# Kernel tuning notes

Hardware: AMD Instinct MI355X
Metric: run time of the kernel (lower is better)

The kernel has to match this reference:

```python
import jax, jax.numpy as jnp
import numpy as np

# Dimensions (see shape_source)
B, L, H, NH = 4, 1024, 768, 12      # batch, seq len, hidden, attention heads
E, MPE, K = 32, 4, 16               # entities/doc, mentions per entity, link spans/doc
EM = E * MPE                        # total mentions per doc
TYPE_DIM = 20
OFFSET = 1                          # bert-style [CLS] offset


def setup_inputs() -> dict:
    key = jax.random.key(0)
    ks = jax.random.split(key, 6)
    sequence_output = jax.random.normal(ks[0], (B, L, H), jnp.float32)
    attention = jax.random.uniform(ks[1], (B, NH, L, L), jnp.float32)
    type_table = jax.random.normal(ks[2], (3, TYPE_DIM), jnp.float32)
    mention_pos = jax.random.randint(ks[3], (B, E, MPE), 0, L - 2)
    link_start = jax.random.randint(ks[4], (B, K), 0, L - 64)
    link_len = jax.random.randint(ks[5], (B, K), 0, 31)
    return dict(sequence_output=sequence_output, attention=attention,
                type_table=type_table, mention_pos=mention_pos,
                link_start=link_start, link_len=link_len)


def reference(sequence_output, attention, type_table, mention_pos, link_start, link_len):
    dt = sequence_output.dtype
    # ---- mention gather (make_graph): mention node = token emb at start+offset ----
    pos = (mention_pos + OFFSET).reshape(B, EM)                       # [B,EM]
    m_emb = jnp.take_along_axis(sequence_output, pos[:, :, None], axis=1)  # [B,EM,H]
    # attention rows at mention positions: [B,NH,EM,L]
    mention_att = jax.vmap(lambda a, p: a[:, p])(attention, pos)
    # ---- entity pooling: logsumexp of member mention embs, mean of their att rows ----
    entity_emb = jax.nn.logsumexp(m_emb.reshape(B, E, MPE, H), axis=2)      # [B,E,H]
    entity_att = mention_att.reshape(B, NH, E, MPE, L).mean(axis=3)         # [B,NH,E,L]
    # ---- link span pooling: mean over rows of (head-mean att[s:e,s:e]) @ seq[s:e] ----
    att_h = attention.mean(axis=1)                                          # [B,L,L]
    s = link_start + OFFSET
    e = link_start + link_len + 1 + OFFSET                                  # span len >= 1
    r = jnp.arange(L)
    mask = ((r[None, None, :] >= s[:, :, None]) & (r[None, None, :] < e[:, :, None])).astype(dt)  # [B,K,L]
    length = (e - s).astype(dt)[:, :, None]
    w = jnp.einsum('bkr,brc->bkc', mask, att_h) * mask                      # row-summed span att
    link_rep = jnp.einsum('bkc,bch->bkh', w, sequence_output) / length      # [B,K,H]
    # ---- node bank: [entities | mentions | links] + type embedding ----
    nodes_raw = jnp.concatenate([entity_emb, m_emb, link_rep], axis=1)      # [B,N,H]
    type_ids = jnp.concatenate([jnp.zeros(E, jnp.int32), jnp.ones(EM, jnp.int32),
                                jnp.full((K,), 2, jnp.int32)])
    nodes_type = jnp.broadcast_to(type_table[type_ids][None], (B, E + EM + K, TYPE_DIM))
    nodes = jnp.concatenate([nodes_raw, nodes_type], axis=-1)               # [B,N,H+20]
    # ---- relation_map: attention-weighted context pooling over the document ----
    e_att = entity_att.mean(axis=1)                                         # [B,E,L] head-mean
    e_att = e_att / (e_att.sum(axis=-1, keepdims=True) + 1e-5)
    e_context = jnp.einsum('bel,blh->beh', e_att, sequence_output)          # [B,E,H]
    m_att = mention_att.mean(axis=1)                                        # [B,EM,L]
    m_att = m_att / (m_att.sum(axis=-1, keepdims=True) + 1e-5)
    m_context = jnp.einsum('bml,blh->bmh', m_att, sequence_output)          # [B,EM,H]
    # pack all outputs into one array (contexts zero-padded to feature dim H+TYPE_DIM)
    ctx = jnp.concatenate([e_context, m_context], axis=1)                   # [B,E+EM,H]
    ctx = jnp.concatenate([ctx, jnp.zeros((B, E + EM, TYPE_DIM), dt)], axis=-1)
    return jnp.concatenate([nodes, ctx], axis=1)                            # [B,N+E+EM,H+20]
```

## Files before the change

kernel.cpp:

```cpp
#include <hip/hip_runtime.h>

constexpr int B = 4, L = 1024, H = 768, NH = 12;
constexpr int E = 32, MPE = 4, K = 16, EM = E * MPE;
constexpr int TYPE_DIM = 20;
constexpr int NNODE = E + EM + K;
constexpr int NROWS = NNODE + E + EM;
constexpr int F = H + TYPE_DIM;
constexpr int NCTX = E + EM;

constexpr int KS = 4;
constexpr int KC = L / KS;
constexpr int RG = 8;
constexpr int CT = 128;
constexpr int NG = NCTX / RG;
constexpr int NT = H / CT;

__global__ __launch_bounds__(512) void k_rows(
        const float* __restrict__ att, const int* __restrict__ mpos,
        float* __restrict__ m_row, float* __restrict__ e_row) {
    int be = blockIdx.x;
    int b = be >> 5;
    int tid = threadIdx.x;
    int c0 = tid * 2;

    int pos[MPE];
    float acc[MPE][2];
#pragma unroll
    for (int mp = 0; mp < MPE; ++mp) {
        pos[mp] = mpos[be * MPE + mp] + 1;
        acc[mp][0] = 0.f; acc[mp][1] = 0.f;
    }
    for (int nh = 0; nh < NH; ++nh) {
#pragma unroll
        for (int mp = 0; mp < MPE; ++mp) {
            const float* row =
                att + (((size_t)(b * NH + nh)) * L + pos[mp]) * L + c0;
            float2 v = *(const float2*)row;
            acc[mp][0] += v.x; acc[mp][1] += v.y;
        }
    }
    float part[MPE];
    float er[2] = {0.f, 0.f};
#pragma unroll
    for (int mp = 0; mp < MPE; ++mp) {
        float s = 0.f;
#pragma unroll
        for (int j = 0; j < 2; ++j) {
            float val = acc[mp][j] * (1.f / NH);
            acc[mp][j] = val; s += val; er[j] += val;
        }
        part[mp] = s;
    }
    __shared__ float red[8][4];
    __shared__ float sinv[5];
    int lane = tid & 63, wid = tid >> 6;
#pragma unroll
    for (int mp = 0; mp < MPE; ++mp) {
        float v = part[mp];
#pragma unroll
        for (int o = 32; o; o >>= 1) v += __shfl_down(v, o, 64);
        if (lane == 0) red[wid][mp] = v;
    }
    __syncthreads();
    if (tid < MPE) {
        float s = 0.f;
#pragma unroll
        for (int w = 0; w < 8; ++w) s += red[w][tid];
        sinv[tid] = 1.f / (s + 1e-5f);
        red[0][tid] = s;
    }
    __syncthreads();
    if (tid == 0) {
        float es = 0.25f * (red[0][0] + red[0][1] + red[0][2] + red[0][3]);
        sinv[4] = 1.f / (es + 1e-5f);
    }
    __syncthreads();
    float einv = sinv[4];
#pragma unroll
    for (int mp = 0; mp < MPE; ++mp) {
        float inv = sinv[mp];
        float2 w;
        w.x = acc[mp][0] * inv; w.y = acc[mp][1] * inv;
        *(float2*)(m_row + ((size_t)(be * MPE + mp)) * L + c0) = w;
    }
    {
        float2 w;
        w.x = 0.25f * er[0] * einv; w.y = 0.25f * er[1] * einv;
        *(float2*)(e_row + (size_t)be * L + c0) = w;
    }
}

__global__ __launch_bounds__(64) void k_ctx(
        const float* __restrict__ seq,
        const float* __restrict__ m_row, const float* __restrict__ e_row,
        float* __restrict__ part) {
    int blk = blockIdx.x;
    int xcd = blk & 7;
    int b = xcd >> 1;
    int idx = ((blk >> 3) << 1) | (xcd & 1);
    int kc = idx & 3;
    int t  = (idx >> 2) % NT;
    int g  = idx / (4 * NT);
    int c = t * CT + (int)threadIdx.x * 2;

    const float* wp[RG];
#pragma unroll
    for (int ri = 0; ri < RG; ++ri) {
        int r = g * RG + ri;
        wp[ri] = ((r < E) ? e_row + ((size_t)(b * E + r)) * L
                          : m_row + ((size_t)(b * EM + (r - E))) * L) + kc * KC;
    }
    const float* sp = seq + ((size_t)b * L + kc * KC) * H + c;

    float acc[RG][2] = {};
    for (int l0 = 0; l0 < KC; l0 += 8) {
        float2 sv[8];
#pragma unroll
        for (int i = 0; i < 8; ++i)
            sv[i] = *(const float2*)(sp + (size_t)(l0 + i) * H);
#pragma unroll
        for (int i = 0; i < 8; ++i) {
#pragma unroll
            for (int ri = 0; ri < RG; ++ri) {
                float w = wp[ri][l0 + i];
                acc[ri][0] += w * sv[i].x;
                acc[ri][1] += w * sv[i].y;
            }
        }
    }
    float* pp = part + (((size_t)kc * B + b) * NCTX + g * RG) * H + c;
#pragma unroll
    for (int ri = 0; ri < RG; ++ri) {
        float2 w; w.x = acc[ri][0]; w.y = acc[ri][1];
        *(float2*)(pp + (size_t)ri * H) = w;
    }
}

__global__ __launch_bounds__(256) void k_assemble(
        const float* __restrict__ seq,
        const float* __restrict__ att,
        const float* __restrict__ ttab,
        const int* __restrict__ mpos,
        const int* __restrict__ lstart, const int* __restrict__ llen,
        const float* __restrict__ part,
        float* __restrict__ out) {
    int blk = blockIdx.x;
    int b = blk / NROWS, r = blk % NROWS;
    int tid = threadIdx.x;
    float* orow = out + ((size_t)b * NROWS + r) * F;

    if (r < E) {
        const int* pp = mpos + (b * E + r) * MPE;
        int p0 = pp[0] + 1, p1 = pp[1] + 1, p2 = pp[2] + 1, p3 = pp[3] + 1;
        const float* sb = seq + (size_t)b * L * H;
#pragma unroll
        for (int j = 0; j < 3; ++j) {
            int h = tid + j * 256;
            float x0 = sb[(size_t)p0 * H + h];
            float x1 = sb[(size_t)p1 * H + h];
            float x2 = sb[(size_t)p2 * H + h];
            float x3 = sb[(size_t)p3 * H + h];
            float mx = fmaxf(fmaxf(x0, x1), fmaxf(x2, x3));
            float sm = expf(x0 - mx) + expf(x1 - mx) + expf(x2 - mx) + expf(x3 - mx);
            orow[h] = mx + logf(sm);
        }
        if (tid < TYPE_DIM) orow[H + tid] = ttab[0 * TYPE_DIM + tid];
    } else if (r < E + EM) {
        int m = r - E;
        int p = mpos[b * EM + m] + 1;
        const float* srow = seq + ((size_t)b * L + p) * H;
#pragma unroll
        for (int j = 0; j < 3; ++j) orow[tid + j * 256] = srow[tid + j * 256];
        if (tid < TYPE_DIM) orow[H + tid] = ttab[1 * TYPE_DIM + tid];
    } else if (r < NNODE) {
        int k = r - (E + EM);
        int s = lstart[b * K + k] + 1;
        int len = llen[b * K + k] + 1;
        int c = tid & 31, sub = tid >> 5;

        __shared__ float partial[8][32];
        __shared__ float wbuf[32];

        float v = 0.f;
        int pairs = len * NH;
        for (int p = sub; p < pairs; p += 8) {
            int rr = s + p / NH;
            int nh = p % NH;
            v += att[(((size_t)(b * NH + nh)) * L + rr) * L + (s + c)];
        }
        partial[sub][c] = v;
        __syncthreads();
        if (tid < 32) {
            float t = 0.f;
#pragma unroll
            for (int q = 0; q < 8; ++q) t += partial[q][tid];
            wbuf[tid] = t * (1.f / NH);
        }
        __syncthreads();

        const float* sb = seq + (size_t)b * L * H;
        float invlen = 1.f / (float)len;
#pragma unroll
        for (int j = 0; j < 3; ++j) {
            int h = tid + j * 256;
            float acc = 0.f;
            for (int cc = 0; cc < len; ++cc)
                acc += wbuf[cc] * sb[(size_t)(s + cc) * H + h];
            orow[h] = acc * invlen;
        }
        if (tid < TYPE_DIM) orow[H + tid] = ttab[2 * TYPE_DIM + tid];
    } else {
        int rr = r - NNODE;
        const float* pp = part + ((size_t)b * NCTX + rr) * H;
#pragma unroll
        for (int j = 0; j < 3; ++j) {
            int h = tid + j * 256;
            float s = 0.f;
#pragma unroll
            for (int kc = 0; kc < KS; ++kc)
                s += pp[(size_t)kc * B * NCTX * H + h];
            orow[h] = s;
        }
        if (tid < TYPE_DIM) orow[H + tid] = 0.f;
    }
}

extern "C" void kernel_launch(void* const* d_in, const int* in_sizes, int n_in,
                              void* d_out, int out_size, void* d_ws, size_t ws_size,
                              hipStream_t stream) {
    const float* seq  = (const float*)d_in[0];
    const float* att  = (const float*)d_in[1];
    const float* ttab = (const float*)d_in[2];
    const int* mpos   = (const int*)d_in[3];
    const int* lstart = (const int*)d_in[4];
    const int* llen   = (const int*)d_in[5];
    float* out = (float*)d_out;

    float* m_row = (float*)d_ws;
    float* e_row = m_row + (size_t)B * EM * L;
    float* part  = e_row + (size_t)B * E * L;

    k_rows<<<B * E, 512, 0, stream>>>(att, mpos, m_row, e_row);
    k_ctx<<<B * NG * NT * KS, 64, 0, stream>>>(seq, m_row, e_row, part);
    k_assemble<<<B * NROWS, 256, 0, stream>>>(seq, att, ttab, mpos,
                                              lstart, llen, part, out);
}
```

Before: 314.5 us.

## Split row kernel, defer normalization to ctx kernel with LDS-staged weights

k_rows now runs two blocks per entity, one per column half, and writes unnormalized rows plus partial sums, which removes two block barriers and gives more parallelism. k_ctx combines the two partial sums to normalize the weights, stages them in LDS, and reads them as float4. Tiles are retuned to 16 rows per group and 8 K-splits. The extra K-splits double the partial buffer that k_assemble reads and sums.

```diff
diff --git a/kernel.cpp b/kernel.cpp
--- a/kernel.cpp
+++ b/kernel.cpp
@@ -8,20 +8,22 @@
 constexpr int F = H + TYPE_DIM;
 constexpr int NCTX = E + EM;
 
-constexpr int KS = 4;
+constexpr int KS = 8;
 constexpr int KC = L / KS;
-constexpr int RG = 8;
+constexpr int RG = 16;
 constexpr int CT = 128;
 constexpr int NG = NCTX / RG;
 constexpr int NT = H / CT;
 
-__global__ __launch_bounds__(512) void k_rows(
+__global__ __launch_bounds__(256) void k_rows(
         const float* __restrict__ att, const int* __restrict__ mpos,
-        float* __restrict__ m_row, float* __restrict__ e_row) {
-    int be = blockIdx.x;
+        float* __restrict__ m_row, float* __restrict__ e_row,
+        float* __restrict__ msum, float* __restrict__ esum) {
+    int blk = blockIdx.x;
+    int be = blk >> 1, half = blk & 1;
     int b = be >> 5;
     int tid = threadIdx.x;
-    int c0 = tid * 2;
+    int c0 = half * 512 + tid * 2;
 
     int pos[MPE];
     float acc[MPE][2];
@@ -51,8 +53,7 @@
         }
         part[mp] = s;
     }
-    __shared__ float red[8][4];
-    __shared__ float sinv[5];
+    __shared__ float red[4][MPE];
     int lane = tid & 63, wid = tid >> 6;
 #pragma unroll
     for (int mp = 0; mp < MPE; ++mp) {
@@ -63,29 +64,23 @@
     }
     __syncthreads();
     if (tid < MPE) {
-        float s = 0.f;
-#pragma unroll
-        for (int w = 0; w < 8; ++w) s += red[w][tid];
-        sinv[tid] = 1.f / (s + 1e-5f);
-        red[0][tid] = s;
-    }
-    __syncthreads();
+        float s = red[0][tid] + red[1][tid] + red[2][tid] + red[3][tid];
+        msum[half * (B * EM) + be * MPE + tid] = s;
+    }
     if (tid == 0) {
-        float es = 0.25f * (red[0][0] + red[0][1] + red[0][2] + red[0][3]);
-        sinv[4] = 1.f / (es + 1e-5f);
-    }
-    __syncthreads();
-    float einv = sinv[4];
-#pragma unroll
-    for (int mp = 0; mp < MPE; ++mp) {
-        float inv = sinv[mp];
-        float2 w;
-        w.x = acc[mp][0] * inv; w.y = acc[mp][1] * inv;
+        float es = 0.f;
+#pragma unroll
+        for (int mp = 0; mp < MPE; ++mp)
+            es += red[0][mp] + red[1][mp] + red[2][mp] + red[3][mp];
+        esum[half * (B * E) + be] = 0.25f * es;
+    }
+#pragma unroll
+    for (int mp = 0; mp < MPE; ++mp) {
+        float2 w; w.x = acc[mp][0]; w.y = acc[mp][1];
         *(float2*)(m_row + ((size_t)(be * MPE + mp)) * L + c0) = w;
     }
     {
-        float2 w;
-        w.x = 0.25f * er[0] * einv; w.y = 0.25f * er[1] * einv;
+        float2 w; w.x = 0.25f * er[0]; w.y = 0.25f * er[1];
         *(float2*)(e_row + (size_t)be * L + c0) = w;
     }
 }
@@ -93,24 +88,40 @@
 __global__ __launch_bounds__(64) void k_ctx(
         const float* __restrict__ seq,
         const float* __restrict__ m_row, const float* __restrict__ e_row,
+        const float* __restrict__ msum, const float* __restrict__ esum,
         float* __restrict__ part) {
     int blk = blockIdx.x;
     int xcd = blk & 7;
     int b = xcd >> 1;
     int idx = ((blk >> 3) << 1) | (xcd & 1);
-    int kc = idx & 3;
-    int t  = (idx >> 2) % NT;
-    int g  = idx / (4 * NT);
-    int c = t * CT + (int)threadIdx.x * 2;
-
-    const float* wp[RG];
-#pragma unroll
-    for (int ri = 0; ri < RG; ++ri) {
-        int r = g * RG + ri;
-        wp[ri] = ((r < E) ? e_row + ((size_t)(b * E + r)) * L
-                          : m_row + ((size_t)(b * EM + (r - E))) * L) + kc * KC;
-    }
-    const float* sp = seq + ((size_t)b * L + kc * KC) * H + c;
+    int kc = idx & 7;
+    int t  = (idx >> 3) % NT;
+    int g  = idx / (8 * NT);
+    int tid = threadIdx.x;
+    int r0 = g * RG;
+
+    __shared__ float w_lds[RG][KC];
+#pragma unroll
+    for (int it = 0; it < RG; ++it) {
+        int r = r0 + it;
+        const float* rp; float s;
+        if (r < E) {
+            rp = e_row + ((size_t)(b * E + r)) * L;
+            s = esum[b * E + r] + esum[B * E + b * E + r];
+        } else {
+            int m = r - E;
+            rp = m_row + ((size_t)(b * EM + m)) * L;
+            s = msum[b * EM + m] + msum[B * EM + b * EM + m];
+        }
+        float inv = 1.f / (s + 1e-5f);
+        float2 v = *(const float2*)(rp + kc * KC + tid * 2);
+        w_lds[it][tid * 2]     = v.x * inv;
+        w_lds[it][tid * 2 + 1] = v.y * inv;
+    }
+    __syncthreads();
+
+    int c = t * CT + tid * 2;
+    const float* sp = seq + ((size_t)(b * L + kc * KC)) * H + c;
 
     float acc[RG][2] = {};
     for (int l0 = 0; l0 < KC; l0 += 8) {
@@ -119,16 +130,20 @@
         for (int i = 0; i < 8; ++i)
             sv[i] = *(const float2*)(sp + (size_t)(l0 + i) * H);
 #pragma unroll
-        for (int i = 0; i < 8; ++i) {
-#pragma unroll
-            for (int ri = 0; ri < RG; ++ri) {
-                float w = wp[ri][l0 + i];
-                acc[ri][0] += w * sv[i].x;
-                acc[ri][1] += w * sv[i].y;
-            }
-        }
-    }
-    float* pp = part + (((size_t)kc * B + b) * NCTX + g * RG) * H + c;
+        for (int ri = 0; ri < RG; ++ri) {
+            float4 w0 = *(const float4*)&w_lds[ri][l0];
+            float4 w1 = *(const float4*)&w_lds[ri][l0 + 4];
+            acc[ri][0] += w0.x * sv[0].x; acc[ri][1] += w0.x * sv[0].y;
+            acc[ri][0] += w0.y * sv[1].x; acc[ri][1] += w0.y * sv[1].y;
+            acc[ri][0] += w0.z * sv[2].x; acc[ri][1] += w0.z * sv[2].y;
+            acc[ri][0] += w0.w * sv[3].x; acc[ri][1] += w0.w * sv[3].y;
+            acc[ri][0] += w1.x * sv[4].x; acc[ri][1] += w1.x * sv[4].y;
+            acc[ri][0] += w1.y * sv[5].x; acc[ri][1] += w1.y * sv[5].y;
+            acc[ri][0] += w1.z * sv[6].x; acc[ri][1] += w1.z * sv[6].y;
+            acc[ri][0] += w1.w * sv[7].x; acc[ri][1] += w1.w * sv[7].y;
+        }
+    }
+    float* pp = part + (((size_t)kc * B + b) * NCTX + r0) * H + c;
 #pragma unroll
     for (int ri = 0; ri < RG; ++ri) {
         float2 w; w.x = acc[ri][0]; w.y = acc[ri][1];
@@ -239,9 +254,11 @@
     float* m_row = (float*)d_ws;
     float* e_row = m_row + (size_t)B * EM * L;
     float* part  = e_row + (size_t)B * E * L;
-
-    k_rows<<<B * E, 512, 0, stream>>>(att, mpos, m_row, e_row);
-    k_ctx<<<B * NG * NT * KS, 64, 0, stream>>>(seq, m_row, e_row, part);
+    float* msum  = part + (size_t)KS * B * NCTX * H;
+    float* esum  = msum + (size_t)2 * B * EM;
+
+    k_rows<<<B * E * 2, 256, 0, stream>>>(att, mpos, m_row, e_row, msum, esum);
+    k_ctx<<<B * NG * NT * KS, 64, 0, stream>>>(seq, m_row, e_row, msum, esum, part);
     k_assemble<<<B * NROWS, 256, 0, stream>>>(seq, att, ttab, mpos,
                                               lstart, llen, part, out);
 }
```

New measurement: 313.5 us. About the same (-0.3%).
